# Performance work log

Hardware: AMD Instinct MI355X
Metric: run time of the kernel (lower is better)

The kernel has to match this reference:

```python
import jax, jax.numpy as jnp
import numpy as np

DIM = 2048
D_INNER = 2048
B = 4
T = 4096
INIT_DECAY = 0.5


def setup_inputs() -> dict:
    key = jax.random.key(0)
    k1, k2, k3 = jax.random.split(key, 3)
    x = jax.random.normal(k1, (B, T, DIM), dtype=jnp.float32)
    h0 = jnp.zeros((B, D_INNER), dtype=jnp.float32)
    # xavier_uniform for Linear(dim -> d_inner) and Linear(d_inner -> dim)
    lim_in = float(np.sqrt(6.0 / (DIM + D_INNER)))
    W_in = jax.random.uniform(k2, (D_INNER, DIM), minval=-lim_in, maxval=lim_in, dtype=jnp.float32)
    lim_out = float(np.sqrt(6.0 / (D_INNER + DIM)))
    W_out = jax.random.uniform(k3, (DIM, D_INNER), minval=-lim_out, maxval=lim_out, dtype=jnp.float32)
    init_log = float(np.log(INIT_DECAY / (1.0 - INIT_DECAY)))  # logit(0.5) = 0
    log_d = jnp.full((D_INNER,), init_log, dtype=jnp.float32)
    b = jnp.zeros((D_INNER,), dtype=jnp.float32)
    return {"x": x, "h0": h0, "W_in": W_in, "W_out": W_out, "log_d": log_d, "b": b}


def reference(x, h0, W_in, W_out, log_d, b):
    # x: [B, T, dim]
    d = jax.nn.sigmoid(log_d)                       # [D] per-dim decay in (0,1)
    xp = jax.nn.silu(jnp.einsum('btd,ed->bte', x, W_in))  # [B, T, D_inner]
    xs = jnp.swapaxes(xp, 0, 1)                     # [T, B, D]

    def step(h_prev, xt):
        h_new = d * (xt + h_prev) + b               # diagonal-decay recurrence
        out = h_new * jax.nn.silu(h_new)            # self-gating
        return h_new, out

    h_final, outs = jax.lax.scan(step, h0, xs)      # outs: [T, B, D]
    cell_out = jnp.swapaxes(outs, 0, 1)             # [B, T, D]
    output = jnp.einsum('bte,de->btd', cell_out, W_out)  # [B, T, dim]
    return output, h_final
```

## Files before the change

kernel.cpp:

```cpp
#include <hip/hip_runtime.h>
#include <hip/hip_bf16.h>

#define DIMV 2048
#define DIV  2048
#define BV   4
#define TV   4096
#define MV   (BV * TV)
#define GK   2048
#define NCH  32
#define CH   128

typedef __bf16 bf16x8 __attribute__((ext_vector_type(8)));
typedef __bf16 bf16x4 __attribute__((ext_vector_type(4)));
typedef float  floatx4 __attribute__((ext_vector_type(4)));

__device__ __forceinline__ void gload_lds16(const void* g, void* l) {
    __builtin_amdgcn_global_load_lds((const __attribute__((address_space(1))) void*)g,
                                     (__attribute__((address_space(3))) void*)l,
                                     16, 0, 0);
}

__global__ __launch_bounds__(256) void cvt_all(const float4* __restrict__ x,
                                               const float4* __restrict__ wi,
                                               const float4* __restrict__ wo,
                                               ushort4* __restrict__ xb,
                                               ushort4* __restrict__ wib,
                                               ushort4* __restrict__ wob) {
    int i = blockIdx.x * 256 + threadIdx.x;
    const float4* src;
    ushort4* dst;
    int off;
    if (i < 8388608)       { src = x;  dst = xb;  off = 0; }
    else if (i < 9437184)  { src = wi; dst = wib; off = 8388608; }
    else                   { src = wo; dst = wob; off = 9437184; }
    float4 v = src[i - off];
    __hip_bfloat16 a = __float2bfloat16(v.x);
    __hip_bfloat16 b = __float2bfloat16(v.y);
    __hip_bfloat16 c = __float2bfloat16(v.z);
    __hip_bfloat16 d = __float2bfloat16(v.w);
    ushort4 o;
    o.x = *(unsigned short*)&a;
    o.y = *(unsigned short*)&b;
    o.z = *(unsigned short*)&c;
    o.w = *(unsigned short*)&d;
    dst[i - off] = o;
}

template <int EPI>
__global__ __launch_bounds__(256) void gemm128_bt(const __hip_bfloat16* __restrict__ A,
                                                  const __hip_bfloat16* __restrict__ Bt,
                                                  float* __restrict__ Cf,
                                                  __hip_bfloat16* __restrict__ Cb) {
    __shared__ __align__(16) short As[128 * 32];
    __shared__ __align__(16) short Bs[128 * 32];

    const int tid  = threadIdx.x;
    const int lane = tid & 63;
    const int wave = tid >> 6;
    const int wm   = (wave >> 1) * 64;
    const int wn   = (wave & 1) * 64;
    const int lr   = lane & 15;
    const int lq   = lane >> 4;

    const int num_n = gridDim.x;
    const int p     = blockIdx.y * num_n + blockIdx.x;
    const int GM    = 8;
    const int grp   = p / (GM * num_n);
    const int rem   = p % (GM * num_n);
    const int m0    = (grp * GM + (rem % GM)) * 128;
    const int n0    = (rem / GM) * 128;

    const int srow = tid >> 2;
    const int scol = (tid & 3) * 8;
    const __hip_bfloat16* Ap0 = A  + (size_t)(m0 + srow) * GK + scol;
    const __hip_bfloat16* Ap1 = Ap0 + (size_t)64 * GK;
    const __hip_bfloat16* Bp0 = Bt + (size_t)(n0 + srow) * GK + scol;
    const __hip_bfloat16* Bp1 = Bp0 + (size_t)64 * GK;

    floatx4 acc[4][4];
#pragma unroll
    for (int i = 0; i < 4; ++i)
#pragma unroll
        for (int j = 0; j < 4; ++j) acc[i][j] = 0.f;

    for (int k0 = 0; k0 < GK; k0 += 32) {
        gload_lds16(Ap0 + k0, &As[tid * 8]);
        gload_lds16(Ap1 + k0, &As[2048 + tid * 8]);
        gload_lds16(Bp0 + k0, &Bs[tid * 8]);
        gload_lds16(Bp1 + k0, &Bs[2048 + tid * 8]);
        __syncthreads();

        bf16x8 af[4], bf[4];
#pragma unroll
        for (int i = 0; i < 4; ++i)
            af[i] = *(const bf16x8*)&As[(wm + i * 16 + lr) * 32 + lq * 8];
#pragma unroll
        for (int j = 0; j < 4; ++j)
            bf[j] = *(const bf16x8*)&Bs[(wn + j * 16 + lr) * 32 + lq * 8];
#pragma unroll
        for (int i = 0; i < 4; ++i)
#pragma unroll
            for (int j = 0; j < 4; ++j)
                acc[i][j] = __builtin_amdgcn_mfma_f32_16x16x32_bf16(af[i], bf[j], acc[i][j], 0, 0, 0);
        __syncthreads();
    }

#pragma unroll
    for (int i = 0; i < 4; ++i) {
#pragma unroll
        for (int r = 0; r < 4; ++r) {
            const int row = m0 + wm + i * 16 + lq * 4 + r;
#pragma unroll
            for (int j = 0; j < 4; ++j) {
                const int col = n0 + wn + j * 16 + lr;
                float v = acc[i][j][r];
                if (EPI == 1) {
                    float s = v / (1.f + __expf(-v));
                    Cb[(size_t)row * DIV + col] = __float2bfloat16(s);
                } else {
                    Cf[(size_t)row * DIMV + col] = v;
                }
            }
        }
    }
}

__global__ __launch_bounds__(256) void scan_carry(const __hip_bfloat16* __restrict__ xp,
                                                  const float* __restrict__ logd,
                                                  const float* __restrict__ bias,
                                                  float* __restrict__ carry) {
    const int eg = blockIdx.x * 256 + threadIdx.x;
    const int e0 = eg * 4;
    const int c = blockIdx.y;
    const int b = blockIdx.z;
    const float4 ld = ((const float4*)logd)[eg];
    const float4 bb = ((const float4*)bias)[eg];
    float dv[4] = {1.f / (1.f + __expf(-ld.x)), 1.f / (1.f + __expf(-ld.y)),
                   1.f / (1.f + __expf(-ld.z)), 1.f / (1.f + __expf(-ld.w))};
    float bv[4] = {bb.x, bb.y, bb.z, bb.w};
    const __hip_bfloat16* p = xp + ((size_t)(b * TV + c * CH)) * DIV + e0;
    float h[4] = {0.f, 0.f, 0.f, 0.f};
#pragma unroll 8
    for (int i = 0; i < CH; ++i) {
        bf16x4 v = *(const bf16x4*)(p + (size_t)i * DIV);
#pragma unroll
        for (int j = 0; j < 4; ++j)
            h[j] = dv[j] * ((float)v[j] + h[j]) + bv[j];
    }
    float4 o = {h[0], h[1], h[2], h[3]};
    *(float4*)&carry[((size_t)b * NCH + c) * DIV + e0] = o;
}

__global__ __launch_bounds__(256) void scan_apply(const __hip_bfloat16* __restrict__ xp,
                                                  const float* __restrict__ logd,
                                                  const float* __restrict__ bias,
                                                  const float* __restrict__ h0,
                                                  const float* __restrict__ carry,
                                                  __hip_bfloat16* __restrict__ cell,
                                                  float* __restrict__ hfin) {
    const int eg = blockIdx.x * 256 + threadIdx.x;
    const int e0 = eg * 4;
    const int c = blockIdx.y;
    const int b = blockIdx.z;
    const float4 ld = ((const float4*)logd)[eg];
    const float4 bb = ((const float4*)bias)[eg];
    float dv[4] = {1.f / (1.f + __expf(-ld.x)), 1.f / (1.f + __expf(-ld.y)),
                   1.f / (1.f + __expf(-ld.z)), 1.f / (1.f + __expf(-ld.w))};
    float bv[4] = {bb.x, bb.y, bb.z, bb.w};
    float dCH[4];
#pragma unroll
    for (int j = 0; j < 4; ++j) dCH[j] = __powf(dv[j], (float)CH);

    float4 H4 = *(const float4*)&h0[(size_t)b * DIV + e0];
    float H[4] = {H4.x, H4.y, H4.z, H4.w};
    for (int j = 0; j < c; ++j) {
        float4 cr = *(const float4*)&carry[((size_t)b * NCH + j) * DIV + e0];
#pragma unroll
        for (int q = 0; q < 4; ++q) H[q] = dCH[q] * H[q] + ((const float*)&cr)[q];
    }

    const size_t base = ((size_t)(b * TV + c * CH)) * DIV + e0;
    float h[4] = {H[0], H[1], H[2], H[3]};
#pragma unroll 4
    for (int i = 0; i < CH; ++i) {
        bf16x4 v = *(const bf16x4*)(xp + base + (size_t)i * DIV);
        ushort4 o;
        unsigned short* op = (unsigned short*)&o;
#pragma unroll
        for (int j = 0; j < 4; ++j) {
            h[j] = dv[j] * ((float)v[j] + h[j]) + bv[j];
            float cv = h[j] * (h[j] / (1.f + __expf(-h[j])));
            __hip_bfloat16 cb = __float2bfloat16(cv);
            op[j] = *(unsigned short*)&cb;
        }
        *(ushort4*)(cell + base + (size_t)i * DIV) = o;
    }
    if (c == NCH - 1) {
        float4 o = {h[0], h[1], h[2], h[3]};
        *(float4*)&hfin[(size_t)b * DIV + e0] = o;
    }
}

extern "C" void kernel_launch(void* const* d_in, const int* in_sizes, int n_in,
                              void* d_out, int out_size, void* d_ws, size_t ws_size,
                              hipStream_t stream) {
    const float* x     = (const float*)d_in[0];
    const float* h0    = (const float*)d_in[1];
    const float* W_in  = (const float*)d_in[2];
    const float* W_out = (const float*)d_in[3];
    const float* log_d = (const float*)d_in[4];
    const float* bias  = (const float*)d_in[5];

    float* out  = (float*)d_out;
    float* hfin = out + (size_t)BV * TV * DIMV;

    char* ws = (char*)d_ws;
    __hip_bfloat16* xb    = (__hip_bfloat16*)ws;
    __hip_bfloat16* cellb = xb;
    __hip_bfloat16* wib   = (__hip_bfloat16*)(ws + 67108864);
    __hip_bfloat16* wob   = (__hip_bfloat16*)(ws + 67108864 + 8388608);
    __hip_bfloat16* xpb   = (__hip_bfloat16*)(ws + 67108864 + 16777216);
    float*          carry = (float*)(ws + 134217728 + 16777216);

    {
        int n4 = 10485760;
        cvt_all<<<n4 / 256, 256, 0, stream>>>((const float4*)x, (const float4*)W_in,
                                              (const float4*)W_out,
                                              (ushort4*)xb, (ushort4*)wib, (ushort4*)wob);
    }

    gemm128_bt<1><<<dim3(DIV / 128, MV / 128), 256, 0, stream>>>(xb, wib, nullptr, xpb);

    scan_carry<<<dim3(DIV / 1024, NCH, BV), 256, 0, stream>>>(xpb, log_d, bias, carry);
    scan_apply<<<dim3(DIV / 1024, NCH, BV), 256, 0, stream>>>(xpb, log_d, bias, h0, carry, cellb, hfin);

    gemm128_bt<0><<<dim3(DIMV / 128, MV / 128), 256, 0, stream>>>(cellb, wob, out, nullptr);
}
```

Measured before the change: 670.2 us.

## Double GEMM K-step to 64 with two LDS panels; shrink scan chunk size

The bf16 MFMA GEMM now loads a K=64 slice per iteration into two 32-wide LDS panels, which halves the number of barrier pairs per tile and gives each wave more MFMA work between syncs. Load addressing is rebuilt per wave so each wave fills 16-row strips of a panel. LDS use doubles to 32KB per block, which may lower occupancy. Separately, the scan chunk constants change from 32 chunks of 128 to 64 chunks of 64, which should give the chunked recurrence more parallelism.

```diff
diff --git a/kernel.cpp b/kernel.cpp
--- a/kernel.cpp
+++ b/kernel.cpp
@@ -7,8 +7,8 @@
 #define TV   4096
 #define MV   (BV * TV)
 #define GK   2048
-#define NCH  32
-#define CH   128
+#define NCH  64
+#define CH   64
 
 typedef __bf16 bf16x8 __attribute__((ext_vector_type(8)));
 typedef __bf16 bf16x4 __attribute__((ext_vector_type(4)));
@@ -51,8 +51,8 @@
                                                   const __hip_bfloat16* __restrict__ Bt,
                                                   float* __restrict__ Cf,
                                                   __hip_bfloat16* __restrict__ Cb) {
-    __shared__ __align__(16) short As[128 * 32];
-    __shared__ __align__(16) short Bs[128 * 32];
+    __shared__ __align__(16) short As[2 * 128 * 32];
+    __shared__ __align__(16) short Bs[2 * 128 * 32];
 
     const int tid  = threadIdx.x;
     const int lane = tid & 63;
@@ -70,12 +70,22 @@
     const int m0    = (grp * GM + (rem % GM)) * 128;
     const int n0    = (rem / GM) * 128;
 
-    const int srow = tid >> 2;
-    const int scol = (tid & 3) * 8;
-    const __hip_bfloat16* Ap0 = A  + (size_t)(m0 + srow) * GK + scol;
-    const __hip_bfloat16* Ap1 = Ap0 + (size_t)64 * GK;
-    const __hip_bfloat16* Bp0 = Bt + (size_t)(n0 + srow) * GK + scol;
-    const __hip_bfloat16* Bp1 = Bp0 + (size_t)64 * GK;
+    const __hip_bfloat16* Aps[4];
+    const __hip_bfloat16* Bps[4];
+    short* Ald[4];
+    short* Bld[4];
+#pragma unroll
+    for (int q = 0; q < 4; ++q) {
+        const int j    = wave * 4 + q;
+        const int pan  = j & 1;
+        const int r0   = (j >> 1) * 16;
+        const int row  = r0 + (lane >> 2);
+        const int col  = pan * 32 + (lane & 3) * 8;
+        Aps[q] = A  + (size_t)(m0 + row) * GK + col;
+        Bps[q] = Bt + (size_t)(n0 + row) * GK + col;
+        Ald[q] = &As[pan * 4096 + r0 * 32 + lane * 8];
+        Bld[q] = &Bs[pan * 4096 + r0 * 32 + lane * 8];
+    }
 
     floatx4 acc[4][4];
 #pragma unroll
@@ -83,25 +93,29 @@
 #pragma unroll
         for (int j = 0; j < 4; ++j) acc[i][j] = 0.f;
 
-    for (int k0 = 0; k0 < GK; k0 += 32) {
-        gload_lds16(Ap0 + k0, &As[tid * 8]);
-        gload_lds16(Ap1 + k0, &As[2048 + tid * 8]);
-        gload_lds16(Bp0 + k0, &Bs[tid * 8]);
-        gload_lds16(Bp1 + k0, &Bs[2048 + tid * 8]);
+    for (int k0 = 0; k0 < GK; k0 += 64) {
+#pragma unroll
+        for (int q = 0; q < 4; ++q) {
+            gload_lds16(Aps[q] + k0, Ald[q]);
+            gload_lds16(Bps[q] + k0, Bld[q]);
+        }
         __syncthreads();
 
-        bf16x8 af[4], bf[4];
-#pragma unroll
-        for (int i = 0; i < 4; ++i)
-            af[i] = *(const bf16x8*)&As[(wm + i * 16 + lr) * 32 + lq * 8];
-#pragma unroll
-        for (int j = 0; j < 4; ++j)
-            bf[j] = *(const bf16x8*)&Bs[(wn + j * 16 + lr) * 32 + lq * 8];
-#pragma unroll
-        for (int i = 0; i < 4; ++i)
+#pragma unroll
+        for (int s = 0; s < 2; ++s) {
+            bf16x8 af[4], bfr[4];
+#pragma unroll
+            for (int i = 0; i < 4; ++i)
+                af[i] = *(const bf16x8*)&As[s * 4096 + (wm + i * 16 + lr) * 32 + lq * 8];
 #pragma unroll
             for (int j = 0; j < 4; ++j)
-                acc[i][j] = __builtin_amdgcn_mfma_f32_16x16x32_bf16(af[i], bf[j], acc[i][j], 0, 0, 0);
+                bfr[j] = *(const bf16x8*)&Bs[s * 4096 + (wn + j * 16 + lr) * 32 + lq * 8];
+#pragma unroll
+            for (int i = 0; i < 4; ++i)
+#pragma unroll
+                for (int j = 0; j < 4; ++j)
+                    acc[i][j] = __builtin_amdgcn_mfma_f32_16x16x32_bf16(af[i], bfr[j], acc[i][j], 0, 0, 0);
+        }
         __syncthreads();
     }
 
```

Result: faster. 614.7 us (-8.3%).
